# Optimization experiments

Measured on AMD Instinct MI355X. Metric: run time of the kernel, lower is better.

The kernel has to match this reference:

```python
import jax, jax.numpy as jnp
import numpy as np
import math

B, S, D, H, K, V, F, L = 16, 512, 768, 12, 64, 64, 3072, 12
VOCAB, MAXLEN, NTYPE = 30522, 512, 2
EPS = 1e-12


def setup_inputs():
    key = jax.random.key(0)
    ks = iter(jax.random.split(key, 32))
    std = 0.02
    n = lambda shape: jax.random.normal(next(ks), shape, dtype=jnp.float32) * std
    inp = {
        'input_ids': jax.random.randint(next(ks), (B, S), 0, VOCAB, dtype=jnp.int32),
        'attention_mask': jnp.ones((B, S), dtype=jnp.int32),
        'word_emb': n((VOCAB, D)),
        'pos_emb': n((MAXLEN, D)),
        'type_emb': n((NTYPE, D)),
        'emb_ln_w': jnp.ones((D,), jnp.float32),
        'emb_ln_b': jnp.zeros((D,), jnp.float32),
        'Wq': n((L, D, H * K)), 'bq': jnp.zeros((L, H * K), jnp.float32),
        'Wk': n((L, D, H * K)), 'bk': jnp.zeros((L, H * K), jnp.float32),
        'Wv': n((L, D, H * V)), 'bv': jnp.zeros((L, H * V), jnp.float32),
        'Wo': n((L, H * V, D)), 'bo': jnp.zeros((L, D), jnp.float32),
        'ln1_w': jnp.ones((L, D), jnp.float32), 'ln1_b': jnp.zeros((L, D), jnp.float32),
        'Wf1': n((L, D, F)), 'bf1': jnp.zeros((L, F), jnp.float32),
        'Wf2': n((L, F, D)), 'bf2': jnp.zeros((L, D), jnp.float32),
        'ln2_w': jnp.ones((L, D), jnp.float32), 'ln2_b': jnp.zeros((L, D), jnp.float32),
    }
    return inp


def _layernorm(x, w, b):
    m = jnp.mean(x, axis=-1, keepdims=True)
    v = jnp.mean(jnp.square(x - m), axis=-1, keepdims=True)
    return (x - m) * jax.lax.rsqrt(v + EPS) * w + b


def _masked_softmax(a, mask4):
    # exact replica of the custom masked_softmax (multiplicative mask + zero-sum guard)
    mv = a * mask4
    mx = jnp.max(mv, axis=-1, keepdims=True)
    ex = jnp.exp(mv - mx) * mask4
    s = jnp.sum(ex, axis=-1, keepdims=True)
    s = s + (s == 0).astype(s.dtype)
    return ex / s


def _encoder(h, mask4, Wq, bq, Wk, bk, Wv, bv, Wo, bo, ln1_w, ln1_b, Wf1, bf1, Wf2, bf2, ln2_w, ln2_b):
    scale = 1.0 / math.sqrt(K)

    def layer(h, p):
        wq, bq_, wk, bk_, wv, bv_, wo, bo_, l1w, l1b, wf1, bf1_, wf2, bf2_, l2w, l2b = p
        q = (h @ wq + bq_).reshape(B, S, H, K).transpose(0, 2, 1, 3)  # [B,H,S,K]
        k = (h @ wk + bk_).reshape(B, S, H, K).transpose(0, 2, 1, 3)
        v = (h @ wv + bv_).reshape(B, S, H, V).transpose(0, 2, 1, 3)
        a = jnp.einsum('bhqk,bhsk->bhqs', q, k) * scale  # [B,H,S,S]
        a = _masked_softmax(a, mask4)
        o = jnp.einsum('bhqs,bhsv->bhqv', a, v).transpose(0, 2, 1, 3).reshape(B, S, H * V)
        o = o @ wo + bo_
        h1 = _layernorm(h + o, l1w, l1b)
        ff = jax.nn.gelu(h1 @ wf1 + bf1_, approximate=False) @ wf2 + bf2_
        return _layernorm(h1 + ff, l2w, l2b), None

    params = (Wq, bq, Wk, bk, Wv, bv, Wo, bo, ln1_w, ln1_b, Wf1, bf1, Wf2, bf2, ln2_w, ln2_b)
    h, _ = jax.lax.scan(layer, h, params)
    return h


def reference(input_ids, attention_mask, word_emb, pos_emb, type_emb, emb_ln_w, emb_ln_b,
              Wq, bq, Wk, bk, Wv, bv, Wo, bo, ln1_w, ln1_b, Wf1, bf1, Wf2, bf2, ln2_w, ln2_b):
    word = word_emb[input_ids]                      # [B,S,D]
    pos = pos_emb[jnp.arange(S)][None, :, :]        # [1,S,D]
    tok = type_emb[0][None, None, :]                # token_type_ids are all zeros
    h = _layernorm(word + pos + tok, emb_ln_w, emb_ln_b)
    h = jax.lax.stop_gradient(h)  # embeddings computed under torch.no_grad()
    mask4 = attention_mask[:, None, None, :].astype(jnp.float32)
    return _encoder(h, mask4, Wq, bq, Wk, bk, Wv, bv, Wo, bo, ln1_w, ln1_b, Wf1, bf1, Wf2, bf2, ln2_w, ln2_b)
```

## Files before the change

### kernel.cpp

```cpp
#include <hip/hip_runtime.h>
#include <cstdint>
#include <cstddef>

typedef _Float16 f16;
typedef unsigned short u16;
typedef _Float16 f16x8 __attribute__((ext_vector_type(8)));
typedef float f32x4 __attribute__((ext_vector_type(4)));

#define DEV __device__ __forceinline__

DEV float b2f(u16 u) { union { float f; unsigned int i; } x; x.i = ((unsigned int)u) << 16; return x.f; }
DEV u16 f2b(float f) {
  union { float f; unsigned int i; } x; x.f = f;
  unsigned int u = x.i;
  return (u16)((u + 0x7FFFu + ((u >> 16) & 1u)) >> 16);
}
DEV float ldf(const void* p, long i, int isb) {
  return isb ? b2f(((const u16*)p)[i]) : ((const float*)p)[i];
}

DEV void gl_lds16(const f16* g, f16* l) {
  __builtin_amdgcn_global_load_lds((const __attribute__((address_space(1))) void*)g,
                                   (__attribute__((address_space(3))) void*)l, 16, 0, 0);
}

__global__ void detect_dtype(const u16* __restrict__ we, int* __restrict__ flag) {
  __shared__ int cnt;
  if (threadIdx.x == 0) cnt = 0;
  __syncthreads();
  int ok = 0;
  for (int i = 0; i < 16; i++) {
    u16 u = we[threadIdx.x * 16 + i];
    int e = (u >> 7) & 0xFF;
    if (e >= 90 && e <= 130) ok++;
  }
  atomicAdd(&cnt, ok);
  __syncthreads();
  if (threadIdx.x == 0) *flag = (cnt > 3481) ? 1 : 0;
}

__global__ __launch_bounds__(256) void transpose_layer(const void* __restrict__ Wq, const void* __restrict__ Wk,
                                                       const void* __restrict__ Wv, const void* __restrict__ Wo,
                                                       const void* __restrict__ Wf1, const void* __restrict__ Wf2,
                                                       f16* __restrict__ wt, int l, const int* __restrict__ dflag) {
  __shared__ f16 tile[32][33];
  int isb = *dflag;
  int bid = blockIdx.x;
  const void* ip;
  f16* op;
  int R, C, rblk, cblk;
  long ioff;
  if (bid < 2304) {
    int which = bid / 576, t = bid % 576;
    R = 768; C = 768;
    cblk = t % 24; rblk = t / 24;
    const void* bases[4] = {Wq, Wk, Wv, Wo};
    ip = bases[which];
    ioff = (long)l * 768 * 768;
    long outs[4] = {0, 589824, 1179648, 1769472};
    op = wt + outs[which];
  } else if (bid < 4608) {
    int t = bid - 2304;
    R = 768; C = 3072;
    cblk = t % 96; rblk = t / 96;
    ip = Wf1; ioff = (long)l * 768 * 3072;
    op = wt + 2359296;
  } else {
    int t = bid - 4608;
    R = 3072; C = 768;
    cblk = t % 24; rblk = t / 24;
    ip = Wf2; ioff = (long)l * 3072 * 768;
    op = wt + 4718592;
  }
  int r0 = rblk * 32, c0 = cblk * 32;
  int tx = threadIdx.x & 31, ty = threadIdx.x >> 5;
  for (int i = 0; i < 4; i++) {
    int r = r0 + ty + 8 * i;
    tile[ty + 8 * i][tx] = (f16)ldf(ip, ioff + (long)r * C + c0 + tx, isb);
  }
  __syncthreads();
  for (int i = 0; i < 4; i++) {
    int c = c0 + ty + 8 * i;
    op[(long)c * R + r0 + tx] = tile[tx][ty + 8 * i];
  }
}

__global__ void prep_bias(const void* bq, const void* bk, const void* bv, const void* bo,
                          const void* bf1, const void* bf2,
                          float* bqkv, float* bo_f, float* bf1f, float* bf2f, const int* dflag) {
  int isb = *dflag;
  int i = blockIdx.x * 256 + threadIdx.x;
  if (i < 12 * 768) {
    int l = i / 768, j = i % 768;
    bqkv[l * 2304 + j] = ldf(bq, i, isb);
    bqkv[l * 2304 + 768 + j] = ldf(bk, i, isb);
    bqkv[l * 2304 + 1536 + j] = ldf(bv, i, isb);
    bo_f[i] = ldf(bo, i, isb);
    bf2f[i] = ldf(bf2, i, isb);
  }
  if (i < 12 * 3072) bf1f[i] = ldf(bf1, i, isb);
}

__global__ __launch_bounds__(256) void embed_ln(const int* __restrict__ ids, const void* __restrict__ we,
                                                const void* __restrict__ pe, const void* __restrict__ te,
                                                const void* __restrict__ lw, const void* __restrict__ lb,
                                                f16* __restrict__ h, const int* __restrict__ dflag) {
  int isb = *dflag;
  int wid = threadIdx.x >> 6, lane = threadIdx.x & 63;
  long t = (long)blockIdx.x * 4 + wid;
  int s = (int)(t & 511);
  long id = ids[t];
  float v[12], s1 = 0.f, s2 = 0.f;
  for (int i = 0; i < 12; i++) {
    int j = i * 64 + lane;
    float f = ldf(we, id * 768 + j, isb) + ldf(pe, (long)s * 768 + j, isb) + ldf(te, j, isb);
    v[i] = f; s1 += f; s2 += f * f;
  }
  for (int d = 1; d < 64; d <<= 1) { s1 += __shfl_xor(s1, d, 64); s2 += __shfl_xor(s2, d, 64); }
  float mean = s1 * (1.f / 768.f);
  float var = fmaxf(s2 * (1.f / 768.f) - mean * mean, 0.f);
  float inv = rsqrtf(var + 1e-12f);
  for (int i = 0; i < 12; i++) {
    int j = i * 64 + lane;
    h[t * 768 + j] = (f16)((v[i] - mean) * inv * ldf(lw, j, isb) + ldf(lb, j, isb));
  }
}

template <int FINAL>
__global__ __launch_bounds__(256) void ln_row(const f16* __restrict__ x, const void* __restrict__ lw,
                                              const void* __restrict__ lb, int l, f16* __restrict__ outf,
                                              void* __restrict__ outg, const int* __restrict__ dflag) {
  int isb = *dflag;
  long poff = (long)l * 768;
  int wid = threadIdx.x >> 6, lane = threadIdx.x & 63;
  long t = (long)blockIdx.x * 4 + wid;
  const f16* xr = x + t * 768;
  float v[12], s1 = 0.f, s2 = 0.f;
  for (int i = 0; i < 12; i++) {
    float f = (float)xr[i * 64 + lane];
    v[i] = f; s1 += f; s2 += f * f;
  }
  for (int d = 1; d < 64; d <<= 1) { s1 += __shfl_xor(s1, d, 64); s2 += __shfl_xor(s2, d, 64); }
  float mean = s1 * (1.f / 768.f);
  float var = fmaxf(s2 * (1.f / 768.f) - mean * mean, 0.f);
  float inv = rsqrtf(var + 1e-12f);
  for (int i = 0; i < 12; i++) {
    int j = i * 64 + lane;
    float o = (v[i] - mean) * inv * ldf(lw, poff + j, isb) + ldf(lb, poff + j, isb);
    long idx = t * 768 + j;
    if (FINAL) {
      if (isb) ((u16*)outg)[idx] = f2b(o);
      else     ((float*)outg)[idx] = o;
    } else {
      outf[idx] = (f16)o;
    }
  }
}

template <int EPI>
__global__ __launch_bounds__(256) void gemm_bt(const f16* __restrict__ A, const f16* __restrict__ Bt,
                                               const float* __restrict__ bias, const f16* __restrict__ resid,
                                               f16* __restrict__ C, int M, int N, int K) {
  __shared__ f16 lA[128 * 32];
  __shared__ f16 lB[128 * 32];
  int tid = threadIdx.x, lane = tid & 63;
  int wid = tid >> 6;
  int lm = lane & 15, quad = lane >> 4;
  int wm = wid & 1, wn = wid >> 1;

  int gx = gridDim.x;
  int nwg = gx * gridDim.y;
  int flat = blockIdx.y * gx + blockIdx.x;
  int wgid = (flat & 7) * (nwg >> 3) + (flat >> 3);
  long m0 = (long)(wgid / gx) * 128, n0 = (long)(wgid % gx) * 128;

  f32x4 acc[4][4];
  for (int i = 0; i < 4; i++) for (int j = 0; j < 4; j++) acc[i][j] = (f32x4){0.f, 0.f, 0.f, 0.f};

  int srow = lane >> 2;
  int scol = (lane & 3) * 8;
  const f16* ap0 = A + (m0 + wid * 32 + srow) * (long)K + scol;
  const f16* bp0 = Bt + (n0 + wid * 32 + srow) * (long)K + scol;
  long stride16 = 16 * (long)K;
  f16* la = lA + wid * 1024;
  f16* lb = lB + wid * 1024;

  for (int kt = 0; kt < K; kt += 32) {
    __syncthreads();
    gl_lds16(ap0 + kt, la);
    gl_lds16(ap0 + stride16 + kt, la + 512);
    gl_lds16(bp0 + kt, lb);
    gl_lds16(bp0 + stride16 + kt, lb + 512);
    __syncthreads();
    f16x8 af[4], bf[4];
    for (int mi = 0; mi < 4; mi++) af[mi] = *(const f16x8*)(lA + (wm * 64 + mi * 16 + lm) * 32 + quad * 8);
    for (int ni = 0; ni < 4; ni++) bf[ni] = *(const f16x8*)(lB + (wn * 64 + ni * 16 + lm) * 32 + quad * 8);
    for (int mi = 0; mi < 4; mi++)
      for (int ni = 0; ni < 4; ni++)
        acc[mi][ni] = __builtin_amdgcn_mfma_f32_16x16x32_f16(af[mi], bf[ni], acc[mi][ni], 0, 0, 0);
  }

  for (int mi = 0; mi < 4; mi++)
    for (int ni = 0; ni < 4; ni++) {
      long row = m0 + wm * 64 + mi * 16 + quad * 4;
      long col = n0 + wn * 64 + ni * 16 + lm;
      float bv = bias[col];
      for (int r = 0; r < 4; r++) {
        long idx = (row + r) * N + col;
        float v = acc[mi][ni][r] + bv;
        if (EPI == 1) v = 0.5f * v * (1.f + erff(v * 0.70710678118654752f));
        if (EPI == 2) v += (float)resid[idx];
        C[idx] = (f16)v;
      }
    }
}

__global__ __launch_bounds__(256) void attn_kern(const f16* __restrict__ qkv, const int* __restrict__ amask,
                                                 f16* __restrict__ out) {
  __shared__ f16 sK[64 * 72];
  __shared__ f16 sV[64 * 72];
  __shared__ f16 sP[4 * 16 * 72];
  __shared__ float sM[64];
  int tid = threadIdx.x, wid = tid >> 6, lane = tid & 63;
  int lm = lane & 15, quad = lane >> 4;
  int qt = blockIdx.x, hh = blockIdx.y, bb = blockIdx.z;
  long tok0 = (long)bb * 512;

  const f16* qrow = qkv + (tok0 + qt * 64 + wid * 16 + lm) * 2304 + hh * 64;
  f16x8 qa0 = *(const f16x8*)(qrow + quad * 8);
  f16x8 qa1 = *(const f16x8*)(qrow + 32 + quad * 8);
  for (int j = 0; j < 8; j++) {
    qa0[j] = (f16)((float)qa0[j] * 0.125f);
    qa1[j] = (f16)((float)qa1[j] * 0.125f);
  }

  f32x4 oAcc[4];
  float mrun[4], lrun[4];
  for (int r = 0; r < 4; r++) { mrun[r] = -1e30f; lrun[r] = 0.f; }
  for (int vt = 0; vt < 4; vt++) oAcc[vt] = (f32x4){0.f, 0.f, 0.f, 0.f};
  f16* sPw = sP + wid * 16 * 72;

  for (int kt = 0; kt < 8; kt++) {
    long j0 = tok0 + kt * 64;
    __syncthreads();
    for (int rr = 0; rr < 2; rr++) {
      int g = rr * 256 + tid;
      int key = g >> 3, dp = (g & 7) * 8;
      *(f16x8*)(sK + key * 72 + dp) = *(const f16x8*)(qkv + (j0 + key) * 2304 + 768 + hh * 64 + dp);
      f16x8 vv = *(const f16x8*)(qkv + (j0 + key) * 2304 + 1536 + hh * 64 + dp);
      for (int j = 0; j < 8; j++) sV[(dp + j) * 72 + key] = vv[j];
    }
    if (tid < 64) sM[tid] = (float)amask[j0 + tid];
    __syncthreads();

    f32x4 sAcc[4];
    for (int nt = 0; nt < 4; nt++) {
      f16x8 b0 = *(const f16x8*)(sK + (nt * 16 + lm) * 72 + quad * 8);
      f16x8 b1 = *(const f16x8*)(sK + (nt * 16 + lm) * 72 + 32 + quad * 8);
      f32x4 z = (f32x4){0.f, 0.f, 0.f, 0.f};
      z = __builtin_amdgcn_mfma_f32_16x16x32_f16(qa0, b0, z, 0, 0, 0);
      z = __builtin_amdgcn_mfma_f32_16x16x32_f16(qa1, b1, z, 0, 0, 0);
      sAcc[nt] = z;
    }
    float mvv[4][4];
    for (int nt = 0; nt < 4; nt++) {
      float m = sM[nt * 16 + lm];
      for (int r = 0; r < 4; r++) mvv[nt][r] = sAcc[nt][r] * m;
    }
    for (int r = 0; r < 4; r++) {
      float mx = fmaxf(fmaxf(mvv[0][r], mvv[1][r]), fmaxf(mvv[2][r], mvv[3][r]));
      for (int d = 1; d < 16; d <<= 1) mx = fmaxf(mx, __shfl_xor(mx, d, 64));
      float mnew = fmaxf(mrun[r], mx);
      float alpha = expf(mrun[r] - mnew);
      mrun[r] = mnew;
      float rs = 0.f;
      for (int nt = 0; nt < 4; nt++) {
        float m = sM[nt * 16 + lm];
        float e = expf(mvv[nt][r] - mnew) * m;
        rs += e;
        sPw[(quad * 4 + r) * 72 + nt * 16 + lm] = (f16)e;
      }
      for (int d = 1; d < 16; d <<= 1) rs += __shfl_xor(rs, d, 64);
      lrun[r] = lrun[r] * alpha + rs;
      for (int vt = 0; vt < 4; vt++) oAcc[vt][r] *= alpha;
    }
    __syncthreads();
    f16x8 pa0 = *(const f16x8*)(sPw + lm * 72 + quad * 8);
    f16x8 pa1 = *(const f16x8*)(sPw + lm * 72 + 32 + quad * 8);
    for (int vt = 0; vt < 4; vt++) {
      f16x8 vb0 = *(const f16x8*)(sV + (vt * 16 + lm) * 72 + quad * 8);
      f16x8 vb1 = *(const f16x8*)(sV + (vt * 16 + lm) * 72 + 32 + quad * 8);
      oAcc[vt] = __builtin_amdgcn_mfma_f32_16x16x32_f16(pa0, vb0, oAcc[vt], 0, 0, 0);
      oAcc[vt] = __builtin_amdgcn_mfma_f32_16x16x32_f16(pa1, vb1, oAcc[vt], 0, 0, 0);
    }
  }
  for (int r = 0; r < 4; r++) {
    float l = lrun[r];
    l += (l == 0.f) ? 1.f : 0.f;
    float inv = 1.f / l;
    long row = tok0 + qt * 64 + wid * 16 + quad * 4 + r;
    for (int vt = 0; vt < 4; vt++)
      out[row * 768 + hh * 64 + vt * 16 + lm] = (f16)(oAcc[vt][r] * inv);
  }
}

extern "C" void kernel_launch(void* const* d_in, const int* in_sizes, int n_in,
                              void* d_out, int out_size, void* d_ws, size_t ws_size,
                              hipStream_t stream) {
  const int* ids   = (const int*)d_in[0];
  const int* amask = (const int*)d_in[1];
  const void* we  = d_in[2];
  const void* pe  = d_in[3];
  const void* te  = d_in[4];
  const void* elw = d_in[5];
  const void* elb = d_in[6];
  const void* Wq  = d_in[7];
  const void* bq  = d_in[8];
  const void* Wk  = d_in[9];
  const void* bk  = d_in[10];
  const void* Wv  = d_in[11];
  const void* bv  = d_in[12];
  const void* Wo  = d_in[13];
  const void* bo  = d_in[14];
  const void* l1w = d_in[15];
  const void* l1b = d_in[16];
  const void* Wf1 = d_in[17];
  const void* bf1 = d_in[18];
  const void* Wf2 = d_in[19];
  const void* bf2 = d_in[20];
  const void* l2w = d_in[21];
  const void* l2b = d_in[22];
  (void)in_sizes; (void)n_in; (void)out_size; (void)ws_size;

  char* p = (char*)d_ws;
  auto alloc = [&](size_t bytes) { char* r = p; p += (bytes + 255) & ~(size_t)255; return r; };
  int* dflag  = (int*)alloc(256);
  f16* wt     = (f16*)alloc(9216ll * 768 * 2);
  float* bqkv = (float*)alloc(12 * 2304 * 4);
  float* bo_f = (float*)alloc(12 * 768 * 4);
  float* bf1f = (float*)alloc(12 * 3072 * 4);
  float* bf2f = (float*)alloc(12 * 768 * 4);
  f16* hbuf  = (f16*)alloc(8192ll * 768 * 2);
  f16* h1buf = (f16*)alloc(8192ll * 768 * 2);
  f16* tmp   = (f16*)alloc(8192ll * 768 * 2);
  f16* big   = (f16*)alloc(8192ll * 3072 * 2);
  f16* qkvb  = big;
  f16* ffn1b = big;
  f16* aobuf = big + 8192ll * 2304;

  detect_dtype<<<1, 256, 0, stream>>>((const u16*)we, dflag);
  prep_bias<<<144, 256, 0, stream>>>(bq, bk, bv, bo, bf1, bf2, bqkv, bo_f, bf1f, bf2f, dflag);
  embed_ln<<<2048, 256, 0, stream>>>(ids, we, pe, te, elw, elb, hbuf, dflag);

  for (int l = 0; l < 12; ++l) {
    transpose_layer<<<6912, 256, 0, stream>>>(Wq, Wk, Wv, Wo, Wf1, Wf2, wt, l, dflag);
    gemm_bt<0><<<dim3(18, 64), 256, 0, stream>>>(hbuf, wt, bqkv + l * 2304,
                                                 nullptr, qkvb, 8192, 2304, 768);
    attn_kern<<<dim3(8, 12, 16), 256, 0, stream>>>(qkvb, amask, aobuf);
    gemm_bt<2><<<dim3(6, 64), 256, 0, stream>>>(aobuf, wt + 1769472, bo_f + l * 768,
                                                hbuf, tmp, 8192, 768, 768);
    ln_row<0><<<2048, 256, 0, stream>>>(tmp, l1w, l1b, l, h1buf, nullptr, dflag);
    gemm_bt<1><<<dim3(24, 64), 256, 0, stream>>>(h1buf, wt + 2359296, bf1f + l * 3072,
                                                 nullptr, ffn1b, 8192, 3072, 768);
    gemm_bt<2><<<dim3(6, 64), 256, 0, stream>>>(ffn1b, wt + 4718592, bf2f + l * 768,
                                                h1buf, tmp, 8192, 768, 3072);
    if (l < 11)
      ln_row<0><<<2048, 256, 0, stream>>>(tmp, l2w, l2b, l, hbuf, nullptr, dflag);
    else
      ln_row<1><<<2048, 256, 0, stream>>>(tmp, l2w, l2b, l, nullptr, d_out, dflag);
  }
}
```

Measured before the change: 4.248 ms.

## Pre-transpose V and stream K/V tiles into swizzled LDS via async loads

A new vtrans kernel writes V transposed into a [head*64+d][token] scratch buffer, reusing the tmp buffer. The attention kernel then loads K and V^T tiles with global_load_lds directly into unpadded LDS. It uses an XOR column swizzle to avoid bank conflicts, replacing the scalar per-element V transpose stores. The kernel also preloads the whole 512-entry mask once, uses __expf, drops a block barrier before the per-wave P reads, and reorders the grid so heads of one batch are adjacent. The cost is an extra kernel launch and a round trip of V through global memory.

```diff
diff --git a/kernel.cpp b/kernel.cpp
--- a/kernel.cpp
+++ b/kernel.cpp
@@ -215,16 +215,38 @@
     }
 }
 
-__global__ __launch_bounds__(256) void attn_kern(const f16* __restrict__ qkv, const int* __restrict__ amask,
-                                                 f16* __restrict__ out) {
-  __shared__ f16 sK[64 * 72];
-  __shared__ f16 sV[64 * 72];
+__global__ __launch_bounds__(256) void vtrans(const f16* __restrict__ qkv, f16* __restrict__ vT) {
+  __shared__ f16 sT[64 * 72];
+  int tid = threadIdx.x;
+  int st = blockIdx.x, hh = blockIdx.y, bb = blockIdx.z;
+  long t0 = (long)bb * 512 + st * 64;
+  int r = tid >> 3, c = tid & 7;
+  const f16* src = qkv + 1536 + (long)hh * 64 + c * 8;
+  *(f16x8*)(sT + r * 72 + c * 8)      = *(const f16x8*)(src + (t0 + r) * 2304);
+  *(f16x8*)(sT + (r + 32) * 72 + c * 8) = *(const f16x8*)(src + (t0 + r + 32) * 2304);
+  __syncthreads();
+  int d = tid >> 2, sq = tid & 3;
+  f16 tmp[16];
+  for (int j = 0; j < 16; j++) tmp[j] = sT[(sq * 16 + j) * 72 + d];
+  f16x8* o = (f16x8*)(vT + ((long)hh * 64 + d) * 8192 + t0 + sq * 16);
+  o[0] = *(f16x8*)(tmp);
+  o[1] = *(f16x8*)(tmp + 8);
+}
+
+__global__ __launch_bounds__(256) void attn_kern(const f16* __restrict__ qkv, const f16* __restrict__ vT,
+                                                 const int* __restrict__ amask, f16* __restrict__ out) {
+  __shared__ f16 sK[64 * 64];
+  __shared__ f16 sVT[64 * 64];
   __shared__ f16 sP[4 * 16 * 72];
-  __shared__ float sM[64];
+  __shared__ float sMall[512];
   int tid = threadIdx.x, wid = tid >> 6, lane = tid & 63;
   int lm = lane & 15, quad = lane >> 4;
-  int qt = blockIdx.x, hh = blockIdx.y, bb = blockIdx.z;
+  int xb = blockIdx.x, qt = blockIdx.y;
+  int hh = xb % 12, bb = xb / 12;
   long tok0 = (long)bb * 512;
+
+  sMall[tid] = (float)amask[tok0 + tid];
+  sMall[tid + 256] = (float)amask[tok0 + 256 + tid];
 
   const f16* qrow = qkv + (tok0 + qt * 64 + wid * 16 + lm) * 2304 + hh * 64;
   f16x8 qa0 = *(const f16x8*)(qrow + quad * 8);
@@ -239,44 +261,49 @@
   for (int r = 0; r < 4; r++) { mrun[r] = -1e30f; lrun[r] = 0.f; }
   for (int vt = 0; vt < 4; vt++) oAcc[vt] = (f32x4){0.f, 0.f, 0.f, 0.f};
   f16* sPw = sP + wid * 16 * 72;
+  int swl = (lm & 7) * 8;
+
+  int i0 = wid * 2;
+  int key0 = lane >> 3;
+  int col = ((lane & 7) ^ (lane >> 3)) * 8;
+  const f16* kb0 = qkv + 768 + (long)hh * 64 + col;
+  const f16* vb0 = vT + ((long)hh * 64) * 8192 + tok0 + col;
 
   for (int kt = 0; kt < 8; kt++) {
     long j0 = tok0 + kt * 64;
     __syncthreads();
-    for (int rr = 0; rr < 2; rr++) {
-      int g = rr * 256 + tid;
-      int key = g >> 3, dp = (g & 7) * 8;
-      *(f16x8*)(sK + key * 72 + dp) = *(const f16x8*)(qkv + (j0 + key) * 2304 + 768 + hh * 64 + dp);
-      f16x8 vv = *(const f16x8*)(qkv + (j0 + key) * 2304 + 1536 + hh * 64 + dp);
-      for (int j = 0; j < 8; j++) sV[(dp + j) * 72 + key] = vv[j];
-    }
-    if (tid < 64) sM[tid] = (float)amask[j0 + tid];
+    for (int ii = 0; ii < 2; ii++) {
+      int i = i0 + ii;
+      int rowi = i * 8 + key0;
+      gl_lds16(kb0 + (j0 + rowi) * 2304, sK + i * 512);
+      gl_lds16(vb0 + (long)rowi * 8192 + kt * 64, sVT + i * 512);
+    }
     __syncthreads();
 
     f32x4 sAcc[4];
     for (int nt = 0; nt < 4; nt++) {
-      f16x8 b0 = *(const f16x8*)(sK + (nt * 16 + lm) * 72 + quad * 8);
-      f16x8 b1 = *(const f16x8*)(sK + (nt * 16 + lm) * 72 + 32 + quad * 8);
+      const f16* kr = sK + (nt * 16 + lm) * 64;
+      f16x8 b0 = *(const f16x8*)(kr + ((quad * 8) ^ swl));
+      f16x8 b1 = *(const f16x8*)(kr + ((32 + quad * 8) ^ swl));
       f32x4 z = (f32x4){0.f, 0.f, 0.f, 0.f};
       z = __builtin_amdgcn_mfma_f32_16x16x32_f16(qa0, b0, z, 0, 0, 0);
       z = __builtin_amdgcn_mfma_f32_16x16x32_f16(qa1, b1, z, 0, 0, 0);
       sAcc[nt] = z;
     }
+    float mk[4];
+    for (int nt = 0; nt < 4; nt++) mk[nt] = sMall[kt * 64 + nt * 16 + lm];
     float mvv[4][4];
-    for (int nt = 0; nt < 4; nt++) {
-      float m = sM[nt * 16 + lm];
-      for (int r = 0; r < 4; r++) mvv[nt][r] = sAcc[nt][r] * m;
-    }
+    for (int nt = 0; nt < 4; nt++)
+      for (int r = 0; r < 4; r++) mvv[nt][r] = sAcc[nt][r] * mk[nt];
     for (int r = 0; r < 4; r++) {
       float mx = fmaxf(fmaxf(mvv[0][r], mvv[1][r]), fmaxf(mvv[2][r], mvv[3][r]));
       for (int d = 1; d < 16; d <<= 1) mx = fmaxf(mx, __shfl_xor(mx, d, 64));
       float mnew = fmaxf(mrun[r], mx);
-      float alpha = expf(mrun[r] - mnew);
+      float alpha = __expf(mrun[r] - mnew);
       mrun[r] = mnew;
       float rs = 0.f;
       for (int nt = 0; nt < 4; nt++) {
-        float m = sM[nt * 16 + lm];
-        float e = expf(mvv[nt][r] - mnew) * m;
+        float e = __expf(mvv[nt][r] - mnew) * mk[nt];
         rs += e;
         sPw[(quad * 4 + r) * 72 + nt * 16 + lm] = (f16)e;
       }
@@ -284,14 +311,14 @@
       lrun[r] = lrun[r] * alpha + rs;
       for (int vt = 0; vt < 4; vt++) oAcc[vt][r] *= alpha;
     }
-    __syncthreads();
     f16x8 pa0 = *(const f16x8*)(sPw + lm * 72 + quad * 8);
     f16x8 pa1 = *(const f16x8*)(sPw + lm * 72 + 32 + quad * 8);
     for (int vt = 0; vt < 4; vt++) {
-      f16x8 vb0 = *(const f16x8*)(sV + (vt * 16 + lm) * 72 + quad * 8);
-      f16x8 vb1 = *(const f16x8*)(sV + (vt * 16 + lm) * 72 + 32 + quad * 8);
-      oAcc[vt] = __builtin_amdgcn_mfma_f32_16x16x32_f16(pa0, vb0, oAcc[vt], 0, 0, 0);
-      oAcc[vt] = __builtin_amdgcn_mfma_f32_16x16x32_f16(pa1, vb1, oAcc[vt], 0, 0, 0);
+      const f16* vr = sVT + (vt * 16 + lm) * 64;
+      f16x8 vb0f = *(const f16x8*)(vr + ((quad * 8) ^ swl));
+      f16x8 vb1f = *(const f16x8*)(vr + ((32 + quad * 8) ^ swl));
+      oAcc[vt] = __builtin_amdgcn_mfma_f32_16x16x32_f16(pa0, vb0f, oAcc[vt], 0, 0, 0);
+      oAcc[vt] = __builtin_amdgcn_mfma_f32_16x16x32_f16(pa1, vb1f, oAcc[vt], 0, 0, 0);
     }
   }
   for (int r = 0; r < 4; r++) {
@@ -356,7 +383,8 @@
     transpose_layer<<<6912, 256, 0, stream>>>(Wq, Wk, Wv, Wo, Wf1, Wf2, wt, l, dflag);
     gemm_bt<0><<<dim3(18, 64), 256, 0, stream>>>(hbuf, wt, bqkv + l * 2304,
                                                  nullptr, qkvb, 8192, 2304, 768);
-    attn_kern<<<dim3(8, 12, 16), 256, 0, stream>>>(qkvb, amask, aobuf);
+    vtrans<<<dim3(8, 12, 16), 256, 0, stream>>>(qkvb, tmp);
+    attn_kern<<<dim3(192, 8), 256, 0, stream>>>(qkvb, tmp, amask, aobuf);
     gemm_bt<2><<<dim3(6, 64), 256, 0, stream>>>(aobuf, wt + 1769472, bo_f + l * 768,
                                                 hbuf, tmp, 8192, 768, 768);
     ln_row<0><<<2048, 256, 0, stream>>>(tmp, l1w, l1b, l, h1buf, nullptr, dflag);
```

After: 3.906 ms. -8.1%, faster.
